# Optimization experiments

Measured on AMD Instinct MI355X. Metric: run time of the kernel, lower is better.

The kernel has to match this reference:

```python
import jax, jax.numpy as jnp
import numpy as np

NUM_EXPERTS = 8
TOP_K = 2
D_HIDDEN = 2048
D_EXPERT = 1024
N_TOKENS = 4096


def setup_inputs() -> dict:
    key = jax.random.key(0)
    ks = jax.random.split(key, 8)
    s_d = 1.0 / np.sqrt(D_HIDDEN).astype(np.float32)
    s_h = 1.0 / np.sqrt(D_EXPERT).astype(np.float32)
    return {
        "x": jax.random.normal(ks[0], (N_TOKENS, D_HIDDEN), jnp.float32),
        "W_g": jax.random.normal(ks[1], (D_HIDDEN, NUM_EXPERTS), jnp.float32) * s_d,
        "W_gate": jax.random.normal(ks[2], (NUM_EXPERTS, D_HIDDEN, D_EXPERT), jnp.float32) * s_d,
        "W_up": jax.random.normal(ks[3], (NUM_EXPERTS, D_HIDDEN, D_EXPERT), jnp.float32) * s_d,
        "W_down": jax.random.normal(ks[4], (NUM_EXPERTS, D_EXPERT, D_HIDDEN), jnp.float32) * s_h,
        "Ws_gate": jax.random.normal(ks[5], (D_HIDDEN, D_EXPERT), jnp.float32) * s_d,
        "Ws_up": jax.random.normal(ks[6], (D_HIDDEN, D_EXPERT), jnp.float32) * s_d,
        "Ws_down": jax.random.normal(ks[7], (D_EXPERT, D_HIDDEN), jnp.float32) * s_h,
    }


def reference(x, W_g, W_gate, W_up, W_down, Ws_gate, Ws_up, Ws_down):
    # Router: softmax logits -> top-k scores/indices (fused_gating_topk)
    probs = jax.nn.softmax(x @ W_g, axis=-1)                      # [N, E]
    scores, idx = jax.lax.top_k(probs, TOP_K)                     # [N, K]
    # Per-(token, expert) combine weight; zero for unrouted experts.
    combine = (jax.nn.one_hot(idx, NUM_EXPERTS, dtype=x.dtype) * scores[..., None]).sum(axis=1)  # [N, E]

    # Routed experts: fused gate/up SiLU with per-token weight scaling, then down-proj.
    gate = jnp.einsum('nd,edh->enh', x, W_gate)                   # [E, N, H]
    up = jnp.einsum('nd,edh->enh', x, W_up)                       # [E, N, H]
    h = jax.nn.silu(gate) * up * combine.T[:, :, None]            # weight=0 kills unrouted tokens
    out = jnp.einsum('enh,ehd->nd', h, W_down)                    # [N, D]

    # Shared expert applied to every token (no routing weight).
    shared = (jax.nn.silu(x @ Ws_gate) * (x @ Ws_up)) @ Ws_down
    return out + shared
```

## Files before the change

### kernel.cpp

```cpp
#include <hip/hip_runtime.h>
#include <cstdint>
#include <cstddef>

#define N_TOK 4096
#define D_HID 2048
#define D_EXP 1024
#define NE 8
#define N_ROUTED (N_TOK * 2)
#define N_ROWS (N_ROUTED + N_TOK)
#define MAX_BLK 112

typedef unsigned short u16;
typedef __bf16 bf16x8 __attribute__((ext_vector_type(8)));
typedef float f32x4 __attribute__((ext_vector_type(4)));

constexpr size_t OFF_XB    = 0;
constexpr size_t OFF_WG    = OFF_XB    + 16777216;
constexpr size_t OFF_WU    = OFF_WG    + 33554432;
constexpr size_t OFF_WD    = OFF_WU    + 33554432;
constexpr size_t OFF_WSG   = OFF_WD    + 33554432;
constexpr size_t OFF_WSU   = OFF_WSG   + 4194304;
constexpr size_t OFF_WSD   = OFF_WSU   + 4194304;
constexpr size_t OFF_H     = OFF_WSD   + 4194304;
constexpr size_t OFF_ROWS  = OFF_H     + 25165824;
constexpr size_t OFF_WSLOT = OFF_ROWS  + 49152;
constexpr size_t OFF_SEG   = OFF_WSLOT + 49152;
constexpr size_t OFF_BLK   = OFF_SEG   + 128;
constexpr size_t OFF_TOPI  = OFF_BLK   + 768;
constexpr size_t OFF_TOPW  = OFF_TOPI  + 32768;
constexpr size_t OFF_INV   = OFF_TOPW  + 32768;
constexpr size_t OFF_H2    = OFF_WG;

__device__ __forceinline__ u16 f32_to_bf16(float f) {
    union { float f; unsigned int u; } c; c.f = f;
    unsigned int u = c.u;
    return (u16)((u + 0x7FFFu + ((u >> 16) & 1u)) >> 16);
}
__device__ __forceinline__ float bf16_to_f32(u16 v) {
    union { unsigned int u; float f; } c; c.u = ((unsigned int)v) << 16;
    return c.f;
}

__device__ __forceinline__ void gld_lds16(const u16* g, u16* l) {
    __builtin_amdgcn_global_load_lds(
        (const __attribute__((address_space(1))) void*)g,
        (__attribute__((address_space(3))) void*)l,
        16, 0, 0);
}

__global__ void cvt_x_kernel(const float* __restrict__ x, u16* __restrict__ xb) {
    size_t i = ((size_t)blockIdx.x * 256 + threadIdx.x) * 8;
    float4 a = *(const float4*)(x + i);
    float4 b = *(const float4*)(x + i + 4);
    union { u16 us[8]; uint4 v; } r;
    r.us[0] = f32_to_bf16(a.x); r.us[1] = f32_to_bf16(a.y);
    r.us[2] = f32_to_bf16(a.z); r.us[3] = f32_to_bf16(a.w);
    r.us[4] = f32_to_bf16(b.x); r.us[5] = f32_to_bf16(b.y);
    r.us[6] = f32_to_bf16(b.z); r.us[7] = f32_to_bf16(b.w);
    *(uint4*)(xb + i) = r.v;
}

__global__ void prep_gu_kernel(const float* __restrict__ Wg, const float* __restrict__ Wu,
                               const float* __restrict__ Wsg, const float* __restrict__ Wsu,
                               u16* __restrict__ Wg_t, u16* __restrict__ Wu_t,
                               u16* __restrict__ Wsg_t, u16* __restrict__ Wsu_t) {
    __shared__ float tile[64][66];
    const int z = blockIdx.z;
    const float* src; u16* dst;
    if (z < 8)        { src = Wg + (size_t)z * (D_HID * D_EXP);       dst = Wg_t + (size_t)z * (D_HID * D_EXP); }
    else if (z < 16)  { src = Wu + (size_t)(z - 8) * (D_HID * D_EXP); dst = Wu_t + (size_t)(z - 8) * (D_HID * D_EXP); }
    else if (z == 16) { src = Wsg; dst = Wsg_t; }
    else              { src = Wsu; dst = Wsu_t; }
    const int c0 = blockIdx.x * 64, r0 = blockIdx.y * 64;
    const int tid = threadIdx.x;
    const int tx = tid & 15, ty = tid >> 4;
#pragma unroll
    for (int i = 0; i < 4; i++) {
        float4 v = *(const float4*)(src + (size_t)(r0 + ty + 16 * i) * D_EXP + c0 + tx * 4);
        tile[ty + 16 * i][tx * 4 + 0] = v.x;
        tile[ty + 16 * i][tx * 4 + 1] = v.y;
        tile[ty + 16 * i][tx * 4 + 2] = v.z;
        tile[ty + 16 * i][tx * 4 + 3] = v.w;
    }
    __syncthreads();
    const int kx = tid & 7, cy = tid >> 3;
#pragma unroll
    for (int j = 0; j < 2; j++) {
        int n = cy + 32 * j;
        union { u16 us[8]; uint4 v; } r;
#pragma unroll
        for (int m = 0; m < 8; m++) r.us[m] = f32_to_bf16(tile[kx * 8 + m][n]);
        *(uint4*)(dst + (size_t)(c0 + n) * D_HID + r0 + kx * 8) = r.v;
    }
}

__global__ void prep_d_kernel(const float* __restrict__ Wd, const float* __restrict__ Wsd,
                              u16* __restrict__ Wd_t, u16* __restrict__ Wsd_t) {
    __shared__ float tile[64][66];
    const int z = blockIdx.z;
    const float* src; u16* dst;
    if (z < 8) { src = Wd + (size_t)z * (D_EXP * D_HID); dst = Wd_t + (size_t)z * (D_EXP * D_HID); }
    else       { src = Wsd; dst = Wsd_t; }
    const int c0 = blockIdx.x * 64, r0 = blockIdx.y * 64;
    const int tid = threadIdx.x;
    const int tx = tid & 15, ty = tid >> 4;
#pragma unroll
    for (int i = 0; i < 4; i++) {
        float4 v = *(const float4*)(src + (size_t)(r0 + ty + 16 * i) * D_HID + c0 + tx * 4);
        tile[ty + 16 * i][tx * 4 + 0] = v.x;
        tile[ty + 16 * i][tx * 4 + 1] = v.y;
        tile[ty + 16 * i][tx * 4 + 2] = v.z;
        tile[ty + 16 * i][tx * 4 + 3] = v.w;
    }
    __syncthreads();
    const int kx = tid & 7, cy = tid >> 3;
#pragma unroll
    for (int j = 0; j < 2; j++) {
        int n = cy + 32 * j;
        union { u16 us[8]; uint4 v; } r;
#pragma unroll
        for (int m = 0; m < 8; m++) r.us[m] = f32_to_bf16(tile[kx * 8 + m][n]);
        *(uint4*)(dst + (size_t)(c0 + n) * D_EXP + r0 + kx * 8) = r.v;
    }
}

__global__ void router_kernel(const float* __restrict__ x, const float* __restrict__ Wg,
                              int* __restrict__ topi, float* __restrict__ topw) {
    const int wave = threadIdx.x >> 6, lane = threadIdx.x & 63;
    const int t = blockIdx.x * 4 + wave;
    const float* xr = x + (size_t)t * D_HID;
    float acc[8] = {0.f, 0.f, 0.f, 0.f, 0.f, 0.f, 0.f, 0.f};
    for (int k = lane; k < D_HID; k += 64) {
        float xv = xr[k];
        float4 w0 = *(const float4*)(Wg + k * 8);
        float4 w1 = *(const float4*)(Wg + k * 8 + 4);
        acc[0] += xv * w0.x; acc[1] += xv * w0.y; acc[2] += xv * w0.z; acc[3] += xv * w0.w;
        acc[4] += xv * w1.x; acc[5] += xv * w1.y; acc[6] += xv * w1.z; acc[7] += xv * w1.w;
    }
#pragma unroll
    for (int e = 0; e < 8; e++)
#pragma unroll
        for (int off = 32; off > 0; off >>= 1)
            acc[e] += __shfl_xor(acc[e], off);
    if (lane == 0) {
        float mx = acc[0];
#pragma unroll
        for (int e = 1; e < 8; e++) mx = fmaxf(mx, acc[e]);
        float p[8], sum = 0.f;
#pragma unroll
        for (int e = 0; e < 8; e++) { p[e] = __expf(acc[e] - mx); sum += p[e]; }
        int i0 = 0; float b0 = p[0];
#pragma unroll
        for (int e = 1; e < 8; e++) if (p[e] > b0) { b0 = p[e]; i0 = e; }
        int i1 = -1; float b1 = -1.f;
#pragma unroll
        for (int e = 0; e < 8; e++) if (e != i0 && p[e] > b1) { b1 = p[e]; i1 = e; }
        float inv = 1.f / sum;
        topi[t * 2] = i0;  topi[t * 2 + 1] = i1;
        topw[t * 2] = b0 * inv; topw[t * 2 + 1] = b1 * inv;
    }
}

__global__ void builder_kernel(const int* __restrict__ topi, const float* __restrict__ topw,
                               int* __restrict__ rows, float* __restrict__ wslot,
                               int* __restrict__ seg, int* __restrict__ blkmap,
                               int* __restrict__ inv) {
    __shared__ int cnt[8], offs[8];
    const int tid = threadIdx.x;
    if (tid < 8) cnt[tid] = 0;
    __syncthreads();
    for (int i = tid; i < N_TOK * 2; i += 256) atomicAdd(&cnt[topi[i]], 1);
    __syncthreads();
    if (tid == 0) {
        int run = 0;
        for (int e = 0; e < 8; e++) {
            offs[e] = run; seg[e] = run; seg[16 + e] = cnt[e]; run += cnt[e];
        }
        seg[8] = N_ROUTED; seg[16 + 8] = N_TOK;
        int nb = 0;
        for (int e = 0; e < 9; e++) {
            int L = (e < 8) ? cnt[e] : N_TOK;
            for (int rb = 0; rb * 128 < L; rb++) blkmap[nb++] = (e << 8) | rb;
        }
        seg[10] = nb;
    }
    __syncthreads();
    for (int i = tid; i < N_TOK * 2; i += 256) {
        int e = topi[i];
        int p = atomicAdd(&offs[e], 1);
        rows[p] = i >> 1;
        wslot[p] = topw[i];
        inv[i] = p;
    }
    for (int t = tid; t < N_TOK; t += 256) {
        rows[N_ROUTED + t] = t;
        wslot[N_ROUTED + t] = 1.0f;
    }
}

__global__ __launch_bounds__(256, 2)
void gemm1_kernel(const u16* __restrict__ xb,
                  const u16* __restrict__ Wg_t, const u16* __restrict__ Wu_t,
                  const u16* __restrict__ Wsg_t, const u16* __restrict__ Wsu_t,
                  const int* __restrict__ rows, const float* __restrict__ wslot,
                  const int* __restrict__ seg, const int* __restrict__ blkmap,
                  u16* __restrict__ h) {
    if ((int)blockIdx.x >= seg[10]) return;
    const int code = blkmap[blockIdx.x];
    const int e = code >> 8, rb = code & 255;
    const int s = seg[e], L = seg[e + 16];
    const u16* Bg = (e < NE) ? Wg_t + (size_t)e * D_EXP * D_HID : Wsg_t;
    const u16* Bu = (e < NE) ? Wu_t + (size_t)e * D_EXP * D_HID : Wsu_t;
    const int cbase = blockIdx.y * 128;

    __shared__ u16 As[128 * 32];
    __shared__ u16 Bgs[128 * 32];
    __shared__ u16 Bus[128 * 32];
    __shared__ int tok_s[128];

    const int tid = threadIdx.x;
    if (tid < 128) {
        int lr = rb * 128 + tid;
        tok_s[tid] = rows[s + (lr < L ? lr : 0)];
    }
    __syncthreads();

    const int lane = tid & 63, wave = tid >> 6;
    const int wm = wave & 1, wn = wave >> 1;
    const int ln = lane & 15, quad = lane >> 4;

    const int lr16 = lane >> 2;
    const int c8 = (lane & 3) * 8;
    const int ra0 = wave * 32 + lr16, ra1 = ra0 + 16;
    const size_t ta0 = (size_t)tok_s[ra0] * D_HID + c8;
    const size_t ta1 = (size_t)tok_s[ra1] * D_HID + c8;
    const u16* pbg0 = Bg + (size_t)(cbase + ra0) * D_HID + c8;
    const u16* pbg1 = Bg + (size_t)(cbase + ra1) * D_HID + c8;
    const u16* pbu0 = Bu + (size_t)(cbase + ra0) * D_HID + c8;
    const u16* pbu1 = Bu + (size_t)(cbase + ra1) * D_HID + c8;
    u16* lA0 = As + (size_t)(wave * 32) * 32;
    u16* lA1 = As + (size_t)(wave * 32 + 16) * 32;
    u16* lG0 = Bgs + (size_t)(wave * 32) * 32;
    u16* lG1 = Bgs + (size_t)(wave * 32 + 16) * 32;
    u16* lU0 = Bus + (size_t)(wave * 32) * 32;
    u16* lU1 = Bus + (size_t)(wave * 32 + 16) * 32;

    f32x4 accg[4][4], accu[4][4];
    const f32x4 zero = {0.f, 0.f, 0.f, 0.f};
#pragma unroll
    for (int i = 0; i < 4; i++)
#pragma unroll
        for (int j = 0; j < 4; j++) { accg[i][j] = zero; accu[i][j] = zero; }

    for (int k0 = 0; k0 < D_HID; k0 += 32) {
        __syncthreads();
        gld_lds16(xb + ta0 + k0, lA0);
        gld_lds16(xb + ta1 + k0, lA1);
        gld_lds16(pbg0 + k0, lG0);
        gld_lds16(pbg1 + k0, lG1);
        gld_lds16(pbu0 + k0, lU0);
        gld_lds16(pbu1 + k0, lU1);
        __syncthreads();
        bf16x8 af[4];
#pragma unroll
        for (int sm = 0; sm < 4; sm++)
            af[sm] = *(const bf16x8*)&As[(wm * 64 + sm * 16 + ln) * 32 + quad * 8];
#pragma unroll
        for (int sn = 0; sn < 4; sn++) {
            const bf16x8 bgf = *(const bf16x8*)&Bgs[(wn * 64 + sn * 16 + ln) * 32 + quad * 8];
            const bf16x8 buf = *(const bf16x8*)&Bus[(wn * 64 + sn * 16 + ln) * 32 + quad * 8];
#pragma unroll
            for (int sm = 0; sm < 4; sm++) {
                accg[sm][sn] = __builtin_amdgcn_mfma_f32_16x16x32_bf16(af[sm], bgf, accg[sm][sn], 0, 0, 0);
                accu[sm][sn] = __builtin_amdgcn_mfma_f32_16x16x32_bf16(af[sm], buf, accu[sm][sn], 0, 0, 0);
            }
        }
    }
#pragma unroll
    for (int sm = 0; sm < 4; sm++) {
#pragma unroll
        for (int r = 0; r < 4; r++) {
            int lrow = rb * 128 + wm * 64 + sm * 16 + quad * 4 + r;
            if (lrow >= L) continue;
            int pos = s + lrow;
            float w = wslot[pos];
#pragma unroll
            for (int sn = 0; sn < 4; sn++) {
                float g = accg[sm][sn][r];
                float u = accu[sm][sn][r];
                float hv = (g / (1.f + __expf(-g))) * u * w;
                int col = cbase + wn * 64 + sn * 16 + ln;
                h[(size_t)pos * D_EXP + col] = f32_to_bf16(hv);
            }
        }
    }
}

__global__ __launch_bounds__(256, 2)
void gemm2_kernel(const u16* __restrict__ h,
                  const u16* __restrict__ Wd_t, const u16* __restrict__ Wsd_t,
                  const int* __restrict__ seg, const int* __restrict__ blkmap,
                  u16* __restrict__ h2) {
    if ((int)blockIdx.x >= seg[10]) return;
    const int code = blkmap[blockIdx.x];
    const int e = code >> 8, rb = code & 255;
    const int s = seg[e], L = seg[e + 16];
    const u16* B = (e < NE) ? Wd_t + (size_t)e * D_HID * D_EXP : Wsd_t;
    const int cbase = blockIdx.y * 128;

    __shared__ u16 As[128 * 32];
    __shared__ u16 Bs[128 * 32];

    const int tid = threadIdx.x;
    const int lane = tid & 63, wave = tid >> 6;
    const int wm = wave & 1, wn = wave >> 1;
    const int ln = lane & 15, quad = lane >> 4;

    const int lr16 = lane >> 2;
    const int c8 = (lane & 3) * 8;
    const int ra0 = wave * 32 + lr16, ra1 = ra0 + 16;
    const u16* pa0 = h + (size_t)(s + rb * 128 + ra0) * D_EXP + c8;
    const u16* pa1 = h + (size_t)(s + rb * 128 + ra1) * D_EXP + c8;
    const u16* pb0 = B + (size_t)(cbase + ra0) * D_EXP + c8;
    const u16* pb1 = B + (size_t)(cbase + ra1) * D_EXP + c8;
    u16* lA0 = As + (size_t)(wave * 32) * 32;
    u16* lA1 = As + (size_t)(wave * 32 + 16) * 32;
    u16* lB0 = Bs + (size_t)(wave * 32) * 32;
    u16* lB1 = Bs + (size_t)(wave * 32 + 16) * 32;

    f32x4 acc[4][4];
    const f32x4 zero = {0.f, 0.f, 0.f, 0.f};
#pragma unroll
    for (int i = 0; i < 4; i++)
#pragma unroll
        for (int j = 0; j < 4; j++) acc[i][j] = zero;

    for (int k0 = 0; k0 < D_EXP; k0 += 32) {
        __syncthreads();
        gld_lds16(pa0 + k0, lA0);
        gld_lds16(pa1 + k0, lA1);
        gld_lds16(pb0 + k0, lB0);
        gld_lds16(pb1 + k0, lB1);
        __syncthreads();
        bf16x8 af[4];
#pragma unroll
        for (int sm = 0; sm < 4; sm++)
            af[sm] = *(const bf16x8*)&As[(wm * 64 + sm * 16 + ln) * 32 + quad * 8];
#pragma unroll
        for (int sn = 0; sn < 4; sn++) {
            const bf16x8 bfg = *(const bf16x8*)&Bs[(wn * 64 + sn * 16 + ln) * 32 + quad * 8];
#pragma unroll
            for (int sm = 0; sm < 4; sm++)
                acc[sm][sn] = __builtin_amdgcn_mfma_f32_16x16x32_bf16(af[sm], bfg, acc[sm][sn], 0, 0, 0);
        }
    }
#pragma unroll
    for (int sm = 0; sm < 4; sm++) {
#pragma unroll
        for (int r = 0; r < 4; r++) {
            int lrow = rb * 128 + wm * 64 + sm * 16 + quad * 4 + r;
            if (lrow >= L) continue;
            size_t slot = (size_t)(s + lrow);
#pragma unroll
            for (int sn = 0; sn < 4; sn++) {
                int col = cbase + wn * 64 + sn * 16 + ln;
                h2[slot * D_HID + col] = f32_to_bf16(acc[sm][sn][r]);
            }
        }
    }
}

__global__ void combine_kernel(const u16* __restrict__ h2, const int* __restrict__ inv,
                               float* __restrict__ out) {
    const int t = blockIdx.x;
    const int d = threadIdx.x * 8;
    const size_t r0 = (size_t)inv[t * 2] * D_HID + d;
    const size_t r1 = (size_t)inv[t * 2 + 1] * D_HID + d;
    const size_t r2 = (size_t)(N_ROUTED + t) * D_HID + d;
    union { uint4 v; u16 us[8]; } a, b, c;
    a.v = *(const uint4*)(h2 + r0);
    b.v = *(const uint4*)(h2 + r1);
    c.v = *(const uint4*)(h2 + r2);
    float4 lo, hi;
    lo.x = bf16_to_f32(a.us[0]) + bf16_to_f32(b.us[0]) + bf16_to_f32(c.us[0]);
    lo.y = bf16_to_f32(a.us[1]) + bf16_to_f32(b.us[1]) + bf16_to_f32(c.us[1]);
    lo.z = bf16_to_f32(a.us[2]) + bf16_to_f32(b.us[2]) + bf16_to_f32(c.us[2]);
    lo.w = bf16_to_f32(a.us[3]) + bf16_to_f32(b.us[3]) + bf16_to_f32(c.us[3]);
    hi.x = bf16_to_f32(a.us[4]) + bf16_to_f32(b.us[4]) + bf16_to_f32(c.us[4]);
    hi.y = bf16_to_f32(a.us[5]) + bf16_to_f32(b.us[5]) + bf16_to_f32(c.us[5]);
    hi.z = bf16_to_f32(a.us[6]) + bf16_to_f32(b.us[6]) + bf16_to_f32(c.us[6]);
    hi.w = bf16_to_f32(a.us[7]) + bf16_to_f32(b.us[7]) + bf16_to_f32(c.us[7]);
    float* o = out + (size_t)t * D_HID + d;
    *(float4*)o = lo;
    *(float4*)(o + 4) = hi;
}

extern "C" void kernel_launch(void* const* d_in, const int* in_sizes, int n_in,
                              void* d_out, int out_size, void* d_ws, size_t ws_size,
                              hipStream_t stream) {
    const float* x       = (const float*)d_in[0];
    const float* W_g     = (const float*)d_in[1];
    const float* W_gate  = (const float*)d_in[2];
    const float* W_up    = (const float*)d_in[3];
    const float* W_down  = (const float*)d_in[4];
    const float* Ws_gate = (const float*)d_in[5];
    const float* Ws_up   = (const float*)d_in[6];
    const float* Ws_down = (const float*)d_in[7];
    float* out = (float*)d_out;
    char* ws = (char*)d_ws;

    u16*   xb    = (u16*)(ws + OFF_XB);
    u16*   Wg_t  = (u16*)(ws + OFF_WG);
    u16*   Wu_t  = (u16*)(ws + OFF_WU);
    u16*   Wd_t  = (u16*)(ws + OFF_WD);
    u16*   Wsg_t = (u16*)(ws + OFF_WSG);
    u16*   Wsu_t = (u16*)(ws + OFF_WSU);
    u16*   Wsd_t = (u16*)(ws + OFF_WSD);
    u16*   h     = (u16*)(ws + OFF_H);
    u16*   h2    = (u16*)(ws + OFF_H2);
    int*   rows  = (int*)(ws + OFF_ROWS);
    float* wslot = (float*)(ws + OFF_WSLOT);
    int*   seg   = (int*)(ws + OFF_SEG);
    int*   blkmap= (int*)(ws + OFF_BLK);
    int*   topi  = (int*)(ws + OFF_TOPI);
    float* topw  = (float*)(ws + OFF_TOPW);
    int*   inv   = (int*)(ws + OFF_INV);

    cvt_x_kernel<<<dim3((N_TOK * D_HID) / (256 * 8)), dim3(256), 0, stream>>>(x, xb);
    prep_gu_kernel<<<dim3(D_EXP / 64, D_HID / 64, 18), dim3(256), 0, stream>>>(
        W_gate, W_up, Ws_gate, Ws_up, Wg_t, Wu_t, Wsg_t, Wsu_t);
    prep_d_kernel<<<dim3(D_HID / 64, D_EXP / 64, 9), dim3(256), 0, stream>>>(
        W_down, Ws_down, Wd_t, Wsd_t);

    router_kernel<<<dim3(N_TOK / 4), dim3(256), 0, stream>>>(x, W_g, topi, topw);
    builder_kernel<<<dim3(1), dim3(256), 0, stream>>>(topi, topw, rows, wslot, seg, blkmap, inv);

    gemm1_kernel<<<dim3(MAX_BLK, D_EXP / 128), dim3(256), 0, stream>>>(
        xb, Wg_t, Wu_t, Wsg_t, Wsu_t, rows, wslot, seg, blkmap, h);
    gemm2_kernel<<<dim3(MAX_BLK, D_HID / 128), dim3(256), 0, stream>>>(
        h, Wd_t, Wsd_t, seg, blkmap, h2);
    combine_kernel<<<dim3(N_TOK), dim3(256), 0, stream>>>(h2, inv, out);
}
```

Baseline: 564.1 us.

## Use 256-row tiles with 4-stage async LDS pipeline in both expert GEMMs

Both grouped GEMMs move to 512-thread blocks covering 256 rows, and gemm2 also covers 256 columns. The single-buffer load/sync/compute loop becomes a 4-deep ring of LDS buffers filled by direct global-to-LDS loads issued three K-steps ahead. Manual vmcnt/lgkmcnt waits, barriers and s_setprio interleave loads with MFMA work, and an XOR swizzle is meant to avoid LDS bank conflicts. The goal is to hide global-load latency and raise data reuse per tile. In exchange, 128KB of LDS per block likely limits occupancy to one block per CU, and partial expert tiles waste more work.

```diff
diff --git a/kernel.cpp b/kernel.cpp
--- a/kernel.cpp
+++ b/kernel.cpp
@@ -8,7 +8,9 @@
 #define NE 8
 #define N_ROUTED (N_TOK * 2)
 #define N_ROWS (N_ROUTED + N_TOK)
-#define MAX_BLK 112
+#define MAX_BLK 56
+#define NT1 (D_HID / 32)
+#define NT2 (D_EXP / 32)
 
 typedef unsigned short u16;
 typedef __bf16 bf16x8 __attribute__((ext_vector_type(8)));
@@ -180,7 +182,7 @@
         int nb = 0;
         for (int e = 0; e < 9; e++) {
             int L = (e < 8) ? cnt[e] : N_TOK;
-            for (int rb = 0; rb * 128 < L; rb++) blkmap[nb++] = (e << 8) | rb;
+            for (int rb = 0; rb * 256 < L; rb++) blkmap[nb++] = (e << 8) | rb;
         }
         seg[10] = nb;
     }
@@ -198,13 +200,15 @@
     }
 }
 
-__global__ __launch_bounds__(256, 2)
+__global__ __launch_bounds__(512, 2)
 void gemm1_kernel(const u16* __restrict__ xb,
                   const u16* __restrict__ Wg_t, const u16* __restrict__ Wu_t,
                   const u16* __restrict__ Wsg_t, const u16* __restrict__ Wsu_t,
                   const int* __restrict__ rows, const float* __restrict__ wslot,
                   const int* __restrict__ seg, const int* __restrict__ blkmap,
                   u16* __restrict__ h) {
+    __shared__ u16 lds[4][16384];
+    __shared__ int tok_s[256];
     if ((int)blockIdx.x >= seg[10]) return;
     const int code = blkmap[blockIdx.x];
     const int e = code >> 8, rb = code & 255;
@@ -212,159 +216,197 @@
     const u16* Bg = (e < NE) ? Wg_t + (size_t)e * D_EXP * D_HID : Wsg_t;
     const u16* Bu = (e < NE) ? Wu_t + (size_t)e * D_EXP * D_HID : Wsu_t;
     const int cbase = blockIdx.y * 128;
-
-    __shared__ u16 As[128 * 32];
-    __shared__ u16 Bgs[128 * 32];
-    __shared__ u16 Bus[128 * 32];
-    __shared__ int tok_s[128];
-
     const int tid = threadIdx.x;
-    if (tid < 128) {
-        int lr = rb * 128 + tid;
+    if (tid < 256) {
+        int lr = rb * 256 + tid;
         tok_s[tid] = rows[s + (lr < L ? lr : 0)];
     }
     __syncthreads();
 
-    const int lane = tid & 63, wave = tid >> 6;
-    const int wm = wave & 1, wn = wave >> 1;
-    const int ln = lane & 15, quad = lane >> 4;
-
-    const int lr16 = lane >> 2;
-    const int c8 = (lane & 3) * 8;
-    const int ra0 = wave * 32 + lr16, ra1 = ra0 + 16;
-    const size_t ta0 = (size_t)tok_s[ra0] * D_HID + c8;
-    const size_t ta1 = (size_t)tok_s[ra1] * D_HID + c8;
-    const u16* pbg0 = Bg + (size_t)(cbase + ra0) * D_HID + c8;
-    const u16* pbg1 = Bg + (size_t)(cbase + ra1) * D_HID + c8;
-    const u16* pbu0 = Bu + (size_t)(cbase + ra0) * D_HID + c8;
-    const u16* pbu1 = Bu + (size_t)(cbase + ra1) * D_HID + c8;
-    u16* lA0 = As + (size_t)(wave * 32) * 32;
-    u16* lA1 = As + (size_t)(wave * 32 + 16) * 32;
-    u16* lG0 = Bgs + (size_t)(wave * 32) * 32;
-    u16* lG1 = Bgs + (size_t)(wave * 32 + 16) * 32;
-    u16* lU0 = Bus + (size_t)(wave * 32) * 32;
-    u16* lU1 = Bus + (size_t)(wave * 32 + 16) * 32;
-
-    f32x4 accg[4][4], accu[4][4];
+    const int l = tid & 63, w = tid >> 6;
+    const int rl = l >> 2;
+    const int cg = (l & 3) ^ ((l >> 3) & 3);
+    const int rowS = w * 16 + rl;
+    const u16* gA0 = xb + (size_t)tok_s[rowS] * D_HID + cg * 8;
+    const u16* gA1 = xb + (size_t)tok_s[128 + rowS] * D_HID + cg * 8;
+    const u16* gBg = Bg + (size_t)(cbase + rowS) * D_HID + cg * 8;
+    const u16* gBu = Bu + (size_t)(cbase + rowS) * D_HID + cg * 8;
+    const int wbase = w * 512;
+
+    const int wm = w & 1, wn = w >> 1;
+    const int ln = l & 15, quad = l >> 4;
+    const int pch = (quad ^ ((ln >> 1) & 3)) * 8;
+    const int aoff = (wm * 128 + ln) * 32 + pch;
+    const int goff = 8192 + (wn * 32 + ln) * 32 + pch;
+
+    f32x4 accg[8][2], accu[8][2];
     const f32x4 zero = {0.f, 0.f, 0.f, 0.f};
 #pragma unroll
-    for (int i = 0; i < 4; i++)
-#pragma unroll
-        for (int j = 0; j < 4; j++) { accg[i][j] = zero; accu[i][j] = zero; }
-
-    for (int k0 = 0; k0 < D_HID; k0 += 32) {
-        __syncthreads();
-        gld_lds16(xb + ta0 + k0, lA0);
-        gld_lds16(xb + ta1 + k0, lA1);
-        gld_lds16(pbg0 + k0, lG0);
-        gld_lds16(pbg1 + k0, lG1);
-        gld_lds16(pbu0 + k0, lU0);
-        gld_lds16(pbu1 + k0, lU1);
-        __syncthreads();
-        bf16x8 af[4];
-#pragma unroll
-        for (int sm = 0; sm < 4; sm++)
-            af[sm] = *(const bf16x8*)&As[(wm * 64 + sm * 16 + ln) * 32 + quad * 8];
-#pragma unroll
-        for (int sn = 0; sn < 4; sn++) {
-            const bf16x8 bgf = *(const bf16x8*)&Bgs[(wn * 64 + sn * 16 + ln) * 32 + quad * 8];
-            const bf16x8 buf = *(const bf16x8*)&Bus[(wn * 64 + sn * 16 + ln) * 32 + quad * 8];
-#pragma unroll
-            for (int sm = 0; sm < 4; sm++) {
-                accg[sm][sn] = __builtin_amdgcn_mfma_f32_16x16x32_bf16(af[sm], bgf, accg[sm][sn], 0, 0, 0);
-                accu[sm][sn] = __builtin_amdgcn_mfma_f32_16x16x32_bf16(af[sm], buf, accu[sm][sn], 0, 0, 0);
+    for (int i = 0; i < 8; i++)
+#pragma unroll
+        for (int j = 0; j < 2; j++) { accg[i][j] = zero; accu[i][j] = zero; }
+
+#define STAGE_A1(t) { u16* dst = &lds[(t) & 3][wbase]; \
+        gld_lds16(gA0 + (t) * 32, dst); \
+        gld_lds16(gA1 + (t) * 32, dst + 4096); }
+#define STAGE_B1(t) { u16* dst = &lds[(t) & 3][8192 + wbase]; \
+        gld_lds16(gBg + (t) * 32, dst); \
+        gld_lds16(gBu + (t) * 32, dst + 4096); }
+
+#define G1_PHASE(P, DO_STAGE) { \
+        bf16x8 af[4], bgf[2], buf_[2]; \
+        _Pragma("unroll") \
+        for (int m = 0; m < 4; m++) af[m] = *(const bf16x8*)(bufp + aoff + ((P) * 4 + m) * 512); \
+        _Pragma("unroll") \
+        for (int n = 0; n < 2; n++) { \
+            bgf[n]  = *(const bf16x8*)(bufp + goff + n * 512); \
+            buf_[n] = *(const bf16x8*)(bufp + goff + 4096 + n * 512); } \
+        DO_STAGE; \
+        __builtin_amdgcn_s_barrier(); \
+        asm volatile("s_waitcnt lgkmcnt(0)" ::: "memory"); \
+        __builtin_amdgcn_sched_barrier(0); \
+        __builtin_amdgcn_s_setprio(1); \
+        _Pragma("unroll") \
+        for (int n = 0; n < 2; n++) \
+        _Pragma("unroll") \
+        for (int m = 0; m < 4; m++) { \
+            accg[(P) * 4 + m][n] = __builtin_amdgcn_mfma_f32_16x16x32_bf16(af[m], bgf[n],  accg[(P) * 4 + m][n], 0, 0, 0); \
+            accu[(P) * 4 + m][n] = __builtin_amdgcn_mfma_f32_16x16x32_bf16(af[m], buf_[n], accu[(P) * 4 + m][n], 0, 0, 0); } \
+        __builtin_amdgcn_s_setprio(0); \
+    }
+
+    STAGE_A1(0); STAGE_B1(0);
+    STAGE_A1(1); STAGE_B1(1);
+    STAGE_A1(2); STAGE_B1(2);
+
+#pragma unroll 1
+    for (int t = 0; t < NT1; ++t) {
+        if (t < NT1 - 2)       asm volatile("s_waitcnt vmcnt(8)" ::: "memory");
+        else if (t == NT1 - 2) asm volatile("s_waitcnt vmcnt(4)" ::: "memory");
+        else                   asm volatile("s_waitcnt vmcnt(0)" ::: "memory");
+        __builtin_amdgcn_s_barrier();
+        __builtin_amdgcn_sched_barrier(0);
+        const u16* bufp = &lds[t & 3][0];
+        G1_PHASE(0, if (t + 3 < NT1) STAGE_A1(t + 3));
+        __builtin_amdgcn_s_barrier();
+        G1_PHASE(1, if (t + 3 < NT1) STAGE_B1(t + 3));
+    }
+#undef G1_PHASE
+#undef STAGE_A1
+#undef STAGE_B1
+
+#pragma unroll
+    for (int m = 0; m < 8; m++) {
+#pragma unroll
+        for (int r = 0; r < 4; r++) {
+            int lrow = rb * 256 + wm * 128 + m * 16 + quad * 4 + r;
+            if (lrow >= L) continue;
+            int pos = s + lrow;
+            float wgt = wslot[pos];
+#pragma unroll
+            for (int n = 0; n < 2; n++) {
+                float g = accg[m][n][r];
+                float u = accu[m][n][r];
+                float hv = (g / (1.f + __expf(-g))) * u * wgt;
+                h[(size_t)pos * D_EXP + cbase + wn * 32 + n * 16 + ln] = f32_to_bf16(hv);
             }
         }
     }
-#pragma unroll
-    for (int sm = 0; sm < 4; sm++) {
-#pragma unroll
-        for (int r = 0; r < 4; r++) {
-            int lrow = rb * 128 + wm * 64 + sm * 16 + quad * 4 + r;
-            if (lrow >= L) continue;
-            int pos = s + lrow;
-            float w = wslot[pos];
-#pragma unroll
-            for (int sn = 0; sn < 4; sn++) {
-                float g = accg[sm][sn][r];
-                float u = accu[sm][sn][r];
-                float hv = (g / (1.f + __expf(-g))) * u * w;
-                int col = cbase + wn * 64 + sn * 16 + ln;
-                h[(size_t)pos * D_EXP + col] = f32_to_bf16(hv);
-            }
-        }
-    }
-}
-
-__global__ __launch_bounds__(256, 2)
+}
+
+__global__ __launch_bounds__(512, 2)
 void gemm2_kernel(const u16* __restrict__ h,
                   const u16* __restrict__ Wd_t, const u16* __restrict__ Wsd_t,
                   const int* __restrict__ seg, const int* __restrict__ blkmap,
                   u16* __restrict__ h2) {
+    __shared__ u16 lds[4][16384];
     if ((int)blockIdx.x >= seg[10]) return;
     const int code = blkmap[blockIdx.x];
     const int e = code >> 8, rb = code & 255;
     const int s = seg[e], L = seg[e + 16];
     const u16* B = (e < NE) ? Wd_t + (size_t)e * D_HID * D_EXP : Wsd_t;
-    const int cbase = blockIdx.y * 128;
-
-    __shared__ u16 As[128 * 32];
-    __shared__ u16 Bs[128 * 32];
-
+    const int cbase = blockIdx.y * 256;
     const int tid = threadIdx.x;
-    const int lane = tid & 63, wave = tid >> 6;
-    const int wm = wave & 1, wn = wave >> 1;
-    const int ln = lane & 15, quad = lane >> 4;
-
-    const int lr16 = lane >> 2;
-    const int c8 = (lane & 3) * 8;
-    const int ra0 = wave * 32 + lr16, ra1 = ra0 + 16;
-    const u16* pa0 = h + (size_t)(s + rb * 128 + ra0) * D_EXP + c8;
-    const u16* pa1 = h + (size_t)(s + rb * 128 + ra1) * D_EXP + c8;
-    const u16* pb0 = B + (size_t)(cbase + ra0) * D_EXP + c8;
-    const u16* pb1 = B + (size_t)(cbase + ra1) * D_EXP + c8;
-    u16* lA0 = As + (size_t)(wave * 32) * 32;
-    u16* lA1 = As + (size_t)(wave * 32 + 16) * 32;
-    u16* lB0 = Bs + (size_t)(wave * 32) * 32;
-    u16* lB1 = Bs + (size_t)(wave * 32 + 16) * 32;
-
-    f32x4 acc[4][4];
+
+    const int l = tid & 63, w = tid >> 6;
+    const int rl = l >> 2;
+    const int cg = (l & 3) ^ ((l >> 3) & 3);
+    const int rowS = w * 16 + rl;
+    const u16* gA0 = h + (size_t)(s + rb * 256 + rowS) * D_EXP + cg * 8;
+    const u16* gA1 = gA0 + (size_t)128 * D_EXP;
+    const u16* gB0 = B + (size_t)(cbase + rowS) * D_EXP + cg * 8;
+    const u16* gB1 = gB0 + (size_t)128 * D_EXP;
+    const int wbase = w * 512;
+
+    const int wm = w & 1, wn = w >> 1;
+    const int ln = l & 15, quad = l >> 4;
+    const int pch = (quad ^ ((ln >> 1) & 3)) * 8;
+    const int aoff = (wm * 128 + ln) * 32 + pch;
+    const int boff = 8192 + (wn * 64 + ln) * 32 + pch;
+
+    f32x4 acc[8][4];
     const f32x4 zero = {0.f, 0.f, 0.f, 0.f};
 #pragma unroll
-    for (int i = 0; i < 4; i++)
+    for (int i = 0; i < 8; i++)
 #pragma unroll
         for (int j = 0; j < 4; j++) acc[i][j] = zero;
 
-    for (int k0 = 0; k0 < D_EXP; k0 += 32) {
-        __syncthreads();
-        gld_lds16(pa0 + k0, lA0);
-        gld_lds16(pa1 + k0, lA1);
-        gld_lds16(pb0 + k0, lB0);
-        gld_lds16(pb1 + k0, lB1);
-        __syncthreads();
-        bf16x8 af[4];
-#pragma unroll
-        for (int sm = 0; sm < 4; sm++)
-            af[sm] = *(const bf16x8*)&As[(wm * 64 + sm * 16 + ln) * 32 + quad * 8];
-#pragma unroll
-        for (int sn = 0; sn < 4; sn++) {
-            const bf16x8 bfg = *(const bf16x8*)&Bs[(wn * 64 + sn * 16 + ln) * 32 + quad * 8];
-#pragma unroll
-            for (int sm = 0; sm < 4; sm++)
-                acc[sm][sn] = __builtin_amdgcn_mfma_f32_16x16x32_bf16(af[sm], bfg, acc[sm][sn], 0, 0, 0);
-        }
-    }
-#pragma unroll
-    for (int sm = 0; sm < 4; sm++) {
+#define STAGE_A2(t) { u16* dst = &lds[(t) & 3][wbase]; \
+        gld_lds16(gA0 + (t) * 32, dst); \
+        gld_lds16(gA1 + (t) * 32, dst + 4096); }
+#define STAGE_B2(t) { u16* dst = &lds[(t) & 3][8192 + wbase]; \
+        gld_lds16(gB0 + (t) * 32, dst); \
+        gld_lds16(gB1 + (t) * 32, dst + 4096); }
+
+#define G2_PHASE(P, DO_STAGE) { \
+        bf16x8 af[4], bf[4]; \
+        _Pragma("unroll") \
+        for (int m = 0; m < 4; m++) af[m] = *(const bf16x8*)(bufp + aoff + ((P) * 4 + m) * 512); \
+        _Pragma("unroll") \
+        for (int n = 0; n < 4; n++) bf[n] = *(const bf16x8*)(bufp + boff + n * 512); \
+        DO_STAGE; \
+        __builtin_amdgcn_s_barrier(); \
+        asm volatile("s_waitcnt lgkmcnt(0)" ::: "memory"); \
+        __builtin_amdgcn_sched_barrier(0); \
+        __builtin_amdgcn_s_setprio(1); \
+        _Pragma("unroll") \
+        for (int n = 0; n < 4; n++) \
+        _Pragma("unroll") \
+        for (int m = 0; m < 4; m++) \
+            acc[(P) * 4 + m][n] = __builtin_amdgcn_mfma_f32_16x16x32_bf16(af[m], bf[n], acc[(P) * 4 + m][n], 0, 0, 0); \
+        __builtin_amdgcn_s_setprio(0); \
+    }
+
+    STAGE_A2(0); STAGE_B2(0);
+    STAGE_A2(1); STAGE_B2(1);
+    STAGE_A2(2); STAGE_B2(2);
+
+#pragma unroll 1
+    for (int t = 0; t < NT2; ++t) {
+        if (t < NT2 - 2)       asm volatile("s_waitcnt vmcnt(8)" ::: "memory");
+        else if (t == NT2 - 2) asm volatile("s_waitcnt vmcnt(4)" ::: "memory");
+        else                   asm volatile("s_waitcnt vmcnt(0)" ::: "memory");
+        __builtin_amdgcn_s_barrier();
+        __builtin_amdgcn_sched_barrier(0);
+        const u16* bufp = &lds[t & 3][0];
+        G2_PHASE(0, if (t + 3 < NT2) STAGE_A2(t + 3));
+        __builtin_amdgcn_s_barrier();
+        G2_PHASE(1, if (t + 3 < NT2) STAGE_B2(t + 3));
+    }
+#undef G2_PHASE
+#undef STAGE_A2
+#undef STAGE_B2
+
+#pragma unroll
+    for (int m = 0; m < 8; m++) {
 #pragma unroll
         for (int r = 0; r < 4; r++) {
-            int lrow = rb * 128 + wm * 64 + sm * 16 + quad * 4 + r;
+            int lrow = rb * 256 + wm * 128 + m * 16 + quad * 4 + r;
             if (lrow >= L) continue;
             size_t slot = (size_t)(s + lrow);
 #pragma unroll
-            for (int sn = 0; sn < 4; sn++) {
-                int col = cbase + wn * 64 + sn * 16 + ln;
-                h2[slot * D_HID + col] = f32_to_bf16(acc[sm][sn][r]);
+            for (int n = 0; n < 4; n++) {
+                h2[slot * D_HID + cbase + wn * 64 + n * 16 + ln] = f32_to_bf16(acc[m][n][r]);
             }
         }
     }
@@ -435,9 +477,9 @@
     router_kernel<<<dim3(N_TOK / 4), dim3(256), 0, stream>>>(x, W_g, topi, topw);
     builder_kernel<<<dim3(1), dim3(256), 0, stream>>>(topi, topw, rows, wslot, seg, blkmap, inv);
 
-    gemm1_kernel<<<dim3(MAX_BLK, D_EXP / 128), dim3(256), 0, stream>>>(
+    gemm1_kernel<<<dim3(MAX_BLK, D_EXP / 128), dim3(512), 0, stream>>>(
         xb, Wg_t, Wu_t, Wsg_t, Wsu_t, rows, wslot, seg, blkmap, h);
-    gemm2_kernel<<<dim3(MAX_BLK, D_HID / 128), dim3(256), 0, stream>>>(
+    gemm2_kernel<<<dim3(MAX_BLK, D_HID / 256), dim3(512), 0, stream>>>(
         h, Wd_t, Wsd_t, seg, blkmap, h2);
     combine_kernel<<<dim3(N_TOK), dim3(256), 0, stream>>>(h2, inv, out);
 }
```

After: 539.6 us. 4.4% less time.
